# Kernel optimization log

Hardware: AMD Instinct MI355X
Metric: run time of the kernel (lower is better)

## Reference

```python
import jax, jax.numpy as jnp
import numpy as np
import math

B, S, D = 2, 2048, 2048
H, KVH, WIN = 16, 4, 256
HD = D // H            # 128
QPER = H // KVH        # 4


def setup_inputs() -> dict:
    key = jax.random.key(0)
    ks = jax.random.split(key, 9)
    s = lambda k, shp: jax.random.normal(k, shp, dtype=jnp.float32) * 0.02
    return {
        "x": jax.random.normal(ks[0], (B, S, D), dtype=jnp.float32),
        "Wq": s(ks[1], (D, D)),            "bq": jnp.zeros((D,), jnp.float32),
        "Wk": s(ks[2], (D, KVH * HD)),      "bk": jnp.zeros((KVH * HD,), jnp.float32),
        "Wv": s(ks[3], (D, KVH * HD)),      "bv": jnp.zeros((KVH * HD,), jnp.float32),
        "Wo": s(ks[4], (D, D)),            "bo": jnp.zeros((D,), jnp.float32),
    }


def reference(x, Wq, bq, Wk, bk, Wv, bv, Wo, bo):
    b, s, _ = x.shape
    # projections
    Q = (x @ Wq + bq).reshape(b, s, H, HD).transpose(0, 2, 1, 3)     # [b,H,s,hd]
    K = (x @ Wk + bk).reshape(b, s, KVH, HD).transpose(0, 2, 1, 3)   # [b,kvh,s,hd]
    V = (x @ Wv + bv).reshape(b, s, KVH, HD).transpose(0, 2, 1, 3)   # [b,kvh,s,hd]
    # GQA grouping: head h = g*QPER + q
    Qg = Q.reshape(b, KVH, QPER, s, HD)                               # [b,g,q,s,hd]
    scores = jnp.einsum('bgqsd,bgtd->bgqst', Qg, K)                   # [b,g,q,s,s]
    i = jnp.arange(s)[:, None]
    j = jnp.arange(s)[None, :]
    keep = (j <= i) & (j >= i - WIN + 1)                              # [s,s]
    scores = jnp.where(keep, scores, -jnp.inf)
    A = jax.nn.softmax(scores / math.sqrt(HD), axis=-1)
    O = jnp.einsum('bgqst,bgtd->bgqsd', A, V)                         # [b,g,q,s,hd]
    O = O.reshape(b, H, s, HD).transpose(0, 2, 1, 3).reshape(b, s, D)
    return O @ Wo + bo
```

## Files before the change

kernel.cpp:

```cpp
#include <hip/hip_runtime.h>
#include <hip/hip_bf16.h>
#include <math.h>

typedef __bf16 bf16_t;
typedef bf16_t bf16x8 __attribute__((ext_vector_type(8)));
typedef bf16_t bf16x4 __attribute__((ext_vector_type(4)));
typedef float  f32x4  __attribute__((ext_vector_type(4)));

#define NB    2
#define SEQ   2048
#define DIM   2048
#define NHEAD 16
#define NKVH  4
#define HDIM  128
#define WINSZ 256
#define KVD   512
#define QKVN  3072
#define MROWS 4096

__device__ __forceinline__ void async_copy16(const void* g, void* lds) {
    __builtin_amdgcn_global_load_lds(
        (const __attribute__((address_space(1))) void*)g,
        (__attribute__((address_space(3))) void*)lds,
        16, 0, 0);
}

__global__ __launch_bounds__(256) void preprocess(
    const float* __restrict__ x,  const float* __restrict__ Wq,
    const float* __restrict__ bq, const float* __restrict__ Wk,
    const float* __restrict__ bk, const float* __restrict__ Wv,
    const float* __restrict__ bv, const float* __restrict__ Wo,
    bf16_t* __restrict__ xb, bf16_t* __restrict__ WqkvT,
    bf16_t* __restrict__ WoT, float* __restrict__ bqkv) {
    __shared__ float tile[32][33];
    const int tid = threadIdx.x;
    int bid = blockIdx.x;
    if (bid < 8192) {
        int i = (bid * 256 + tid) * 4;
        float4 v = *(const float4*)(x + i);
        bf16x4 o;
        o[0] = (bf16_t)v.x; o[1] = (bf16_t)v.y; o[2] = (bf16_t)v.z; o[3] = (bf16_t)v.w;
        *(bf16x4*)(xb + i) = o;
        return;
    }
    bid -= 8192;
    const float* src; bf16_t* dst; int N;
    if (bid < 4096)       { src = Wq; dst = WqkvT;                          N = DIM; }
    else if (bid < 5120)  { src = Wk; dst = WqkvT + (size_t)DIM * DIM;      N = KVD; bid -= 4096; }
    else if (bid < 6144)  { src = Wv; dst = WqkvT + (size_t)(DIM+KVD)*DIM;  N = KVD; bid -= 5120; }
    else if (bid < 10240) { src = Wo; dst = WoT;                            N = DIM; bid -= 6144; }
    else {
        int i = (bid - 10240) * 256 + tid;
        if (i < QKVN) {
            float v = (i < DIM) ? bq[i] : ((i < DIM + KVD) ? bk[i - DIM] : bv[i - DIM - KVD]);
            bqkv[i] = v;
        }
        return;
    }
    const int K = DIM;
    int ntile = N / 32;
    int n0 = (bid % ntile) * 32, k0 = (bid / ntile) * 32;
    int tx = tid & 31, ty = tid >> 5;
    for (int r = ty; r < 32; r += 8)
        tile[r][tx] = src[(size_t)(k0 + r) * N + n0 + tx];
    __syncthreads();
    for (int r = ty; r < 32; r += 8)
        dst[(size_t)(n0 + r) * K + k0 + tx] = (bf16_t)tile[tx][r];
}

template <int BM, int BN, int MPOS, typename OutT, bool VFUSE>
__global__ __launch_bounds__(512, 1) void gemm1b(const bf16_t* __restrict__ A,
                                                 const bf16_t* __restrict__ Bt,
                                                 const float* __restrict__ bias,
                                                 OutT* __restrict__ C,
                                                 bf16_t* __restrict__ vtb,
                                                 int M, int N, int K, float qs, int qcols) {
    constexpr int NPOS = 8 / MPOS;
    constexpr int ASLOTS = BM / 16;
    constexpr int BSLOTS = BN / 16;
    constexpr int MF = BM / MPOS / 16;
    constexpr int NF = BN / NPOS / 16;
    constexpr int AHALF = BM * 32;
    constexpr int BHALF = BN * 32;
    constexpr int BUFSZ = 2 * (AHALF + BHALF);
    __shared__ bf16_t lds[2 * BUFSZ];

    const int tid  = threadIdx.x;
    const int wave = tid >> 6;
    const int lane = tid & 63;
    const int lg = lane >> 4, lc = lane & 15;
    const int wr = wave / NPOS, wc = wave % NPOS;

    const int nbn  = N / BN;
    const int nblk = (M / BM) * nbn;
    const int qq   = nblk >> 3;
    const int swz  = (blockIdx.x & 7) * qq + (blockIdx.x >> 3);
    const long brow = (long)(swz / nbn) * BM;
    const long bcol = (long)(swz % nbn) * BN;

    f32x4 acc[MF][NF] = {};

    auto stage = [&](int buf, int p, int kt) {
        const int kcol = kt * 64 + p * 32;
        const int srow = lane >> 2;
        const int sch  = lane & 3;
        {
            bf16_t* d = lds + buf * BUFSZ + p * AHALF;
#pragma unroll
            for (int s = wave; s < ASLOTS; s += 8) {
                int row = s * 16 + srow;
                int ch  = sch ^ ((row >> 1) & 3);
                async_copy16(A + (brow + row) * (long)K + kcol + ch * 8, d + s * 512);
            }
        }
        {
            bf16_t* d = lds + buf * BUFSZ + 2 * AHALF + p * BHALF;
#pragma unroll
            for (int s = wave; s < BSLOTS; s += 8) {
                int row = s * 16 + srow;
                int ch  = sch ^ ((row >> 1) & 3);
                async_copy16(Bt + (bcol + row) * (long)K + kcol + ch * 8, d + s * 512);
            }
        }
    };

    stage(0, 0, 0);
    stage(0, 1, 0);

    const int NT = K >> 6;
    const int cswz = (lg ^ ((lc >> 1) & 3)) * 8;
    for (int t = 0; t < NT; ++t) {
        asm volatile("s_waitcnt vmcnt(0)" ::: "memory");
        __builtin_amdgcn_s_barrier();
        asm volatile("" ::: "memory");
        const bf16_t* base = lds + (t & 1) * BUFSZ;
#pragma unroll
        for (int p = 0; p < 2; ++p) {
            const bf16_t* Ab = base + p * AHALF;
            const bf16_t* Bb = base + 2 * AHALF + p * BHALF;
            bf16x8 af[MF], bv[NF];
#pragma unroll
            for (int m = 0; m < MF; ++m)
                af[m] = *(const bf16x8*)(Ab + (wr * (BM / MPOS) + m * 16 + lc) * 32 + cswz);
#pragma unroll
            for (int n = 0; n < NF; ++n)
                bv[n] = *(const bf16x8*)(Bb + (wc * (BN / NPOS) + n * 16 + lc) * 32 + cswz);
            if (t + 1 < NT) stage((t + 1) & 1, p, t + 1);
#pragma unroll
            for (int m = 0; m < MF; ++m)
#pragma unroll
                for (int n = 0; n < NF; ++n)
                    acc[m][n] = __builtin_amdgcn_mfma_f32_16x16x32_bf16(af[m], bv[n], acc[m][n], 0, 0, 0);
        }
    }

#pragma unroll
    for (int n = 0; n < NF; ++n) {
        int gc = (int)bcol + wc * (BN / NPOS) + n * 16 + lc;
        float bvs = bias[gc];
        if constexpr (VFUSE) {
            if (gc >= DIM + KVD) {
                int vg = (gc - (DIM + KVD)) >> 7;
                int dl = (gc - (DIM + KVD)) & 127;
#pragma unroll
                for (int m = 0; m < MF; ++m) {
                    long gr = brow + wr * (BM / MPOS) + m * 16 + 4 * lg;
                    int bb = (int)(gr >> 11);
                    int js = (int)(gr & (SEQ - 1));
                    bf16x4 ov;
#pragma unroll
                    for (int r = 0; r < 4; ++r) ov[r] = (bf16_t)(acc[m][n][r] + bvs);
                    *(bf16x4*)(vtb + (((size_t)(bb * NKVH) + vg) * 64 + (js >> 5)) * 4096
                                   + dl * 32 + (js & 31)) = ov;
                }
                continue;
            }
        }
        bool ds = gc < qcols;
#pragma unroll
        for (int m = 0; m < MF; ++m) {
            long gr = brow + wr * (BM / MPOS) + m * 16 + 4 * lg;
#pragma unroll
            for (int r = 0; r < 4; ++r) {
                float v = acc[m][n][r] + bvs;
                if (ds) v *= qs;
                C[(gr + r) * (long)N + gc] = (OutT)v;
            }
        }
    }
}

template <int BM, int BN, typename OutT>
__global__ __launch_bounds__(512, 1) void gemm8p(const bf16_t* __restrict__ A,
                                                 const bf16_t* __restrict__ Bt,
                                                 const float* __restrict__ bias,
                                                 OutT* __restrict__ C,
                                                 int M, int N, int K, float qs, int qcols) {
    constexpr int ASLOTS = BM / 16;
    constexpr int BSLOTS = BN / 16;
    constexpr int MF   = BM / 32;
    constexpr int NF   = BN / 64;
    constexpr int AHALF = BM * 32;
    constexpr int BHALF = BN * 32;
    constexpr int BUFSZ = 2 * (AHALF + BHALF);
    __shared__ bf16_t lds[2 * BUFSZ];

    const int tid  = threadIdx.x;
    const int wave = tid >> 6;
    const int lane = tid & 63;
    const int lg = lane >> 4, lc = lane & 15;
    const int wr = wave >> 2, wc = wave & 3;

    const int nbn  = N / BN;
    const int nblk = (M / BM) * nbn;
    const int qq   = nblk >> 3;
    const int swz  = (blockIdx.x & 7) * qq + (blockIdx.x >> 3);
    const long brow = (long)(swz / nbn) * BM;
    const long bcol = (long)(swz % nbn) * BN;

    const int aiss = (ASLOTS - wave + 7) >> 3;
    const int biss = (BSLOTS - wave + 7) >> 3;
    const int miss = aiss + biss;

    f32x4 acc[MF][NF] = {};

    auto stage = [&](int buf, int p, int kt) {
        const int kcol = kt * 64 + p * 32;
        const int srow = lane >> 2;
        const int sch  = lane & 3;
        {
            bf16_t* d = lds + buf * BUFSZ + p * AHALF;
#pragma unroll
            for (int s = wave; s < ASLOTS; s += 8) {
                int row = s * 16 + srow;
                int ch  = sch ^ ((row >> 1) & 3);
                async_copy16(A + (brow + row) * (long)K + kcol + ch * 8, d + s * 512);
            }
        }
        {
            bf16_t* d = lds + buf * BUFSZ + 2 * AHALF + p * BHALF;
#pragma unroll
            for (int s = wave; s < BSLOTS; s += 8) {
                int row = s * 16 + srow;
                int ch  = sch ^ ((row >> 1) & 3);
                async_copy16(Bt + (bcol + row) * (long)K + kcol + ch * 8, d + s * 512);
            }
        }
    };

    stage(0, 0, 0);
    stage(0, 1, 0);

    const int NT = K >> 6;
    const int cswz = (lg ^ ((lc >> 1) & 3)) * 8;
    for (int t = 0; t < NT; ++t) {
#pragma unroll
        for (int p = 0; p < 2; ++p) {
            if (t == NT - 1 && p == 1) {
                asm volatile("s_waitcnt vmcnt(0)" ::: "memory");
            } else if (miss == 4) {
                asm volatile("s_waitcnt vmcnt(4)" ::: "memory");
            } else if (miss == 3) {
                asm volatile("s_waitcnt vmcnt(3)" ::: "memory");
            } else {
                asm volatile("s_waitcnt vmcnt(2)" ::: "memory");
            }
            __builtin_amdgcn_s_barrier();
            asm volatile("" ::: "memory");
            const bf16_t* Ab = lds + (t & 1) * BUFSZ + p * AHALF;
            const bf16_t* Bb = lds + (t & 1) * BUFSZ + 2 * AHALF + p * BHALF;
            bf16x8 af[MF], bv[NF];
#pragma unroll
            for (int m = 0; m < MF; ++m)
                af[m] = *(const bf16x8*)(Ab + (wr * (BM / 2) + m * 16 + lc) * 32 + cswz);
#pragma unroll
            for (int n = 0; n < NF; ++n)
                bv[n] = *(const bf16x8*)(Bb + (wc * (BN / 4) + n * 16 + lc) * 32 + cswz);
            if (t + 1 < NT) stage((t + 1) & 1, p, t + 1);
            __builtin_amdgcn_s_setprio(1);
#pragma unroll
            for (int m = 0; m < MF; ++m)
#pragma unroll
                for (int n = 0; n < NF; ++n)
                    acc[m][n] = __builtin_amdgcn_mfma_f32_16x16x32_bf16(af[m], bv[n], acc[m][n], 0, 0, 0);
            __builtin_amdgcn_s_setprio(0);
        }
    }

#pragma unroll
    for (int n = 0; n < NF; ++n) {
        int gc = (int)bcol + wc * (BN / 4) + n * 16 + lc;
        float bvs = bias[gc];
        bool ds = gc < qcols;
#pragma unroll
        for (int m = 0; m < MF; ++m) {
            long gr = brow + wr * (BM / 2) + m * 16 + 4 * lg;
#pragma unroll
            for (int r = 0; r < 4; ++r) {
                float v = acc[m][n][r] + bvs;
                if (ds) v *= qs;
                C[(gr + r) * (long)N + gc] = (OutT)v;
            }
        }
    }
}

__global__ __launch_bounds__(256) void attn_kernel(const bf16_t* __restrict__ QKV,
                                                   const bf16_t* __restrict__ Vtb,
                                                   bf16_t* __restrict__ Ob) {
    __shared__ bf16_t Kls[3][32 * 128];
    __shared__ bf16_t Vls[3][128 * 32];
    __shared__ bf16_t Pls[4][32 * 40];

    const int wv   = threadIdx.x >> 6;
    const int lane = threadIdx.x & 63;
    const int lg = lane >> 4, lc = lane & 15;

    const int swb = (blockIdx.x & 7) * 64 + (blockIdx.x >> 3);
    const int ti = swb & 63;
    const int g  = (swb >> 6) & 3;
    const int b  = swb >> 8;
    const int h  = g * 4 + wv;
    const int i0 = ti * 32;
    bf16_t* P = &Pls[wv][0];

    bf16x8 qf[2][4];
#pragma unroll
    for (int sq = 0; sq < 2; ++sq) {
        const bf16_t* qp = QKV + ((size_t)(b * SEQ) + i0 + sq * 16 + lc) * QKVN + h * HDIM + lg * 8;
#pragma unroll
        for (int kk = 0; kk < 4; ++kk) qf[sq][kk] = *(const bf16x8*)(qp + kk * 32);
    }

    auto stage = [&](int buf, int jb) {
        const int j0s = jb * 32;
        const bf16_t* kgb = QKV + ((size_t)(b * SEQ) + j0s) * QKVN + DIM + g * HDIM;
#pragma unroll
        for (int ii = 0; ii < 2; ++ii) {
            int i = wv * 2 + ii;
            int row = i * 4 + (lane >> 4);
            int ch  = (lane & 15) ^ (row & 7);
            async_copy16(kgb + (size_t)row * QKVN + ch * 8, &Kls[buf][i * 512]);
        }
        const bf16_t* vgb = Vtb + (((size_t)(b * NKVH) + g) * 64 + jb) * 4096;
#pragma unroll
        for (int ii = 0; ii < 2; ++ii) {
            int i = wv * 2 + ii;
            int row = i * 16 + (lane >> 2);
            int ch  = (lane & 3) ^ ((row ^ (row >> 2)) & 3);
            async_copy16(vgb + row * 32 + ch * 8, &Vls[buf][i * 512]);
        }
    };

    float m_run[2] = {-1e30f, -1e30f}, l_run[2] = {0.f, 0.f};
    f32x4 oacc[2][8] = {};

    int jlo = i0 - (WINSZ - 1); if (jlo < 0) jlo = 0;
    const int jb0 = jlo >> 5;
    const int jb1 = (i0 + 31) >> 5;

    stage(0, jb0);
    if (jb0 + 1 <= jb1) stage(1, jb0 + 1);

    for (int jb = jb0; jb <= jb1; ++jb) {
        const int j0 = jb * 32;
        const int it = jb - jb0;
        const int cur = it % 3;
        if (jb < jb1) asm volatile("s_waitcnt vmcnt(4)" ::: "memory");
        else          asm volatile("s_waitcnt vmcnt(0)" ::: "memory");
        __builtin_amdgcn_s_barrier();
        asm volatile("" ::: "memory");

        bf16x8 kf[2][4];
#pragma unroll
        for (int t = 0; t < 2; ++t)
#pragma unroll
            for (int kk = 0; kk < 4; ++kk) {
                int row = t * 16 + lc;
                int ch  = (kk * 4 + lg) ^ (row & 7);
                kf[t][kk] = *(const bf16x8*)(&Kls[cur][row * 128 + ch * 8]);
            }
        if (jb + 2 <= jb1) stage((it + 2) % 3, jb + 2);
        asm volatile("s_waitcnt lgkmcnt(0)" ::: "memory");
        __builtin_amdgcn_sched_barrier(0);

        f32x4 s[2][2];
        __builtin_amdgcn_s_setprio(1);
#pragma unroll
        for (int t = 0; t < 2; ++t)
#pragma unroll
            for (int sq = 0; sq < 2; ++sq) {
                f32x4 sv = {};
#pragma unroll
                for (int kk = 0; kk < 4; ++kk)
                    sv = __builtin_amdgcn_mfma_f32_16x16x32_bf16(kf[t][kk], qf[sq][kk], sv, 0, 0, 0);
                s[t][sq] = sv;
            }
        __builtin_amdgcn_s_setprio(0);

        const bool edge = (j0 < i0 - (WINSZ - 32)) || (j0 > i0 - 31);
        if (edge) {
#pragma unroll
            for (int t = 0; t < 2; ++t)
#pragma unroll
                for (int sq = 0; sq < 2; ++sq) {
                    int irow = i0 + sq * 16 + lc;
#pragma unroll
                    for (int r = 0; r < 4; ++r) {
                        int j = j0 + t * 16 + 4 * lg + r;
                        if (j > irow || j < irow - (WINSZ - 1)) s[t][sq][r] = -1e30f;
                    }
                }
        }
        float tmax[2];
#pragma unroll
        for (int sq = 0; sq < 2; ++sq) {
            float tm = fmaxf(fmaxf(fmaxf(s[0][sq][0], s[0][sq][1]), fmaxf(s[0][sq][2], s[0][sq][3])),
                             fmaxf(fmaxf(s[1][sq][0], s[1][sq][1]), fmaxf(s[1][sq][2], s[1][sq][3])));
            tm = fmaxf(tm, __shfl_xor(tm, 16, 64));
            tm = fmaxf(tm, __shfl_xor(tm, 32, 64));
            tmax[sq] = tm;
        }
        if (!__all(tmax[0] - m_run[0] <= 8.0f && tmax[1] - m_run[1] <= 8.0f)) {
#pragma unroll
            for (int sq = 0; sq < 2; ++sq) {
                float m_new = fmaxf(m_run[sq], tmax[sq]);
                float resc = __builtin_amdgcn_exp2f(m_run[sq] - m_new);
                l_run[sq] *= resc;
#pragma unroll
                for (int c = 0; c < 8; ++c) {
                    oacc[sq][c][0] *= resc; oacc[sq][c][1] *= resc;
                    oacc[sq][c][2] *= resc; oacc[sq][c][3] *= resc;
                }
                m_run[sq] = m_new;
            }
        }
        float psum[2] = {0.f, 0.f};
#pragma unroll
        for (int t = 0; t < 2; ++t)
#pragma unroll
            for (int sq = 0; sq < 2; ++sq) {
                bf16x4 pk;
#pragma unroll
                for (int r = 0; r < 4; ++r) {
                    float sv = s[t][sq][r];
                    float p = (edge && sv < -5e29f) ? 0.f : __builtin_amdgcn_exp2f(sv - m_run[sq]);
                    psum[sq] += p;
                    pk[r] = (bf16_t)p;
                }
                *(bf16x4*)(P + (sq * 16 + lc) * 40 + t * 16 + lg * 4) = pk;
            }
#pragma unroll
        for (int sq = 0; sq < 2; ++sq) {
            float ps = psum[sq];
            ps += __shfl_xor(ps, 16, 64);
            ps += __shfl_xor(ps, 32, 64);
            l_run[sq] += ps;
        }
        asm volatile("" ::: "memory");

        bf16x8 vf[8];
#pragma unroll
        for (int c = 0; c < 8; ++c) {
            int row = c * 16 + lc;
            int ch  = lg ^ ((row ^ (row >> 2)) & 3);
            vf[c] = *(const bf16x8*)(&Vls[cur][row * 32 + ch * 8]);
        }
        bf16x8 pf[2];
#pragma unroll
        for (int sq = 0; sq < 2; ++sq)
            pf[sq] = *(const bf16x8*)(P + (sq * 16 + lc) * 40 + lg * 8);

        __builtin_amdgcn_s_setprio(1);
#pragma unroll
        for (int c = 0; c < 8; ++c)
#pragma unroll
            for (int sq = 0; sq < 2; ++sq)
                oacc[sq][c] = __builtin_amdgcn_mfma_f32_16x16x32_bf16(vf[c], pf[sq], oacc[sq][c], 0, 0, 0);
        __builtin_amdgcn_s_setprio(0);
    }

#pragma unroll
    for (int sq = 0; sq < 2; ++sq) {
        const float inv = 1.f / l_run[sq];
#pragma unroll
        for (int c = 0; c < 8; ++c) {
            bf16x4 ov;
#pragma unroll
            for (int r = 0; r < 4; ++r) ov[r] = (bf16_t)(oacc[sq][c][r] * inv);
            *(bf16x4*)(Ob + ((size_t)(b * SEQ) + i0 + sq * 16 + lc) * DIM + h * HDIM + c * 16 + lg * 4) = ov;
        }
    }
}

extern "C" void kernel_launch(void* const* d_in, const int* in_sizes, int n_in,
                              void* d_out, int out_size, void* d_ws, size_t ws_size,
                              hipStream_t stream) {
    const float* x  = (const float*)d_in[0];
    const float* Wq = (const float*)d_in[1];
    const float* bq = (const float*)d_in[2];
    const float* Wk = (const float*)d_in[3];
    const float* bk = (const float*)d_in[4];
    const float* Wv = (const float*)d_in[5];
    const float* bv = (const float*)d_in[6];
    const float* Wo = (const float*)d_in[7];
    const float* bo = (const float*)d_in[8];
    float* out = (float*)d_out;

    char* ws = (char*)d_ws;
    bf16_t* xb    = (bf16_t*)(ws);
    bf16_t* WqkvT = (bf16_t*)(ws + (16u << 20));
    bf16_t* WoT   = (bf16_t*)(ws + (28u << 20));
    bf16_t* QKVb  = (bf16_t*)(ws + (36u << 20));
    float*  bqkv  = (float*) (ws + (60u << 20));
    bf16_t* Vtb   = (bf16_t*)(ws + (61u << 20));
    bf16_t* Ob    = xb;

    const float qs = 0.12751707498038074f;

    preprocess<<<18444, 256, 0, stream>>>(x, Wq, bq, Wk, bk, Wv, bv, Wo,
                                          xb, WqkvT, WoT, bqkv);

    gemm1b<256, 192, 4, bf16_t, true><<<dim3((MROWS / 256) * (QKVN / 192)), 512, 0, stream>>>(
        xb, WqkvT, bqkv, QKVb, Vtb, MROWS, QKVN, DIM, qs, DIM);

    attn_kernel<<<dim3(NB * NKVH * (SEQ / 32)), 256, 0, stream>>>(QKVb, Vtb, Ob);

    gemm8p<128, 256, float><<<dim3((MROWS / 128) * (DIM / 256)), 512, 0, stream>>>(
        Ob, WoT, bo, out, MROWS, DIM, DIM, 1.0f, 0);
}
```

Baseline: 139.7 us.

## Triple-buffer output GEMM and double attention query tile per block

The output-projection GEMM now keeps a three-stage LDS ring, prefetching two k-tiles ahead. It waits at one barrier per k-tile instead of one per half-tile and drops the setprio hints. The attention kernel now runs 8 waves over 64 query rows per block, so each staged K/V tile is shared by two query sub-tiles and per-block K/V loads are halved. The costs are more LDS per GEMM block, extra wasted key blocks at the window edges for the first query sub-tile, and a barrier now shared by 8 waves.

New measurement: 139.0 us, median of 2. About the same (-0.5%).

```diff
diff --git a/kernel.cpp b/kernel.cpp
--- a/kernel.cpp
+++ b/kernel.cpp
@@ -190,26 +190,27 @@
     }
 }
 
-template <int BM, int BN, typename OutT>
-__global__ __launch_bounds__(512, 1) void gemm8p(const bf16_t* __restrict__ A,
-                                                 const bf16_t* __restrict__ Bt,
-                                                 const float* __restrict__ bias,
-                                                 OutT* __restrict__ C,
-                                                 int M, int N, int K, float qs, int qcols) {
+template <int BM, int BN, int MPOS, typename OutT>
+__global__ __launch_bounds__(512, 1) void gemm1b3(const bf16_t* __restrict__ A,
+                                                  const bf16_t* __restrict__ Bt,
+                                                  const float* __restrict__ bias,
+                                                  OutT* __restrict__ C,
+                                                  int M, int N, int K, float qs, int qcols) {
+    constexpr int NPOS = 8 / MPOS;
     constexpr int ASLOTS = BM / 16;
     constexpr int BSLOTS = BN / 16;
-    constexpr int MF   = BM / 32;
-    constexpr int NF   = BN / 64;
+    constexpr int MF = BM / MPOS / 16;
+    constexpr int NF = BN / NPOS / 16;
     constexpr int AHALF = BM * 32;
     constexpr int BHALF = BN * 32;
     constexpr int BUFSZ = 2 * (AHALF + BHALF);
-    __shared__ bf16_t lds[2 * BUFSZ];
+    __shared__ bf16_t lds[3 * BUFSZ];
 
     const int tid  = threadIdx.x;
     const int wave = tid >> 6;
     const int lane = tid & 63;
     const int lg = lane >> 4, lc = lane & 15;
-    const int wr = wave >> 2, wc = wave & 3;
+    const int wr = wave / NPOS, wc = wave % NPOS;
 
     const int nbn  = N / BN;
     const int nblk = (M / BM) * nbn;
@@ -220,7 +221,7 @@
 
     const int aiss = (ASLOTS - wave + 7) >> 3;
     const int biss = (BSLOTS - wave + 7) >> 3;
-    const int miss = aiss + biss;
+    const int m2   = 2 * (aiss + biss);
 
     f32x4 acc[MF][NF] = {};
 
@@ -250,51 +251,47 @@
 
     stage(0, 0, 0);
     stage(0, 1, 0);
+    stage(1, 0, 1);
+    stage(1, 1, 1);
 
     const int NT = K >> 6;
     const int cswz = (lg ^ ((lc >> 1) & 3)) * 8;
     for (int t = 0; t < NT; ++t) {
+        if (t == NT - 1)      asm volatile("s_waitcnt vmcnt(0)" ::: "memory");
+        else if (m2 == 6)     asm volatile("s_waitcnt vmcnt(6)" ::: "memory");
+        else if (m2 == 8)     asm volatile("s_waitcnt vmcnt(8)" ::: "memory");
+        else                  asm volatile("s_waitcnt vmcnt(4)" ::: "memory");
+        __builtin_amdgcn_s_barrier();
+        asm volatile("" ::: "memory");
+        const bf16_t* base = lds + (t % 3) * BUFSZ;
 #pragma unroll
         for (int p = 0; p < 2; ++p) {
-            if (t == NT - 1 && p == 1) {
-                asm volatile("s_waitcnt vmcnt(0)" ::: "memory");
-            } else if (miss == 4) {
-                asm volatile("s_waitcnt vmcnt(4)" ::: "memory");
-            } else if (miss == 3) {
-                asm volatile("s_waitcnt vmcnt(3)" ::: "memory");
-            } else {
-                asm volatile("s_waitcnt vmcnt(2)" ::: "memory");
-            }
-            __builtin_amdgcn_s_barrier();
-            asm volatile("" ::: "memory");
-            const bf16_t* Ab = lds + (t & 1) * BUFSZ + p * AHALF;
-            const bf16_t* Bb = lds + (t & 1) * BUFSZ + 2 * AHALF + p * BHALF;
+            const bf16_t* Ab = base + p * AHALF;
+            const bf16_t* Bb = base + 2 * AHALF + p * BHALF;
             bf16x8 af[MF], bv[NF];
 #pragma unroll
             for (int m = 0; m < MF; ++m)
-                af[m] = *(const bf16x8*)(Ab + (wr * (BM / 2) + m * 16 + lc) * 32 + cswz);
+                af[m] = *(const bf16x8*)(Ab + (wr * (BM / MPOS) + m * 16 + lc) * 32 + cswz);
 #pragma unroll
             for (int n = 0; n < NF; ++n)
-                bv[n] = *(const bf16x8*)(Bb + (wc * (BN / 4) + n * 16 + lc) * 32 + cswz);
-            if (t + 1 < NT) stage((t + 1) & 1, p, t + 1);
-            __builtin_amdgcn_s_setprio(1);
+                bv[n] = *(const bf16x8*)(Bb + (wc * (BN / NPOS) + n * 16 + lc) * 32 + cswz);
+            if (t + 2 < NT) stage((t + 2) % 3, p, t + 2);
 #pragma unroll
             for (int m = 0; m < MF; ++m)
 #pragma unroll
                 for (int n = 0; n < NF; ++n)
                     acc[m][n] = __builtin_amdgcn_mfma_f32_16x16x32_bf16(af[m], bv[n], acc[m][n], 0, 0, 0);
-            __builtin_amdgcn_s_setprio(0);
         }
     }
 
 #pragma unroll
     for (int n = 0; n < NF; ++n) {
-        int gc = (int)bcol + wc * (BN / 4) + n * 16 + lc;
+        int gc = (int)bcol + wc * (BN / NPOS) + n * 16 + lc;
         float bvs = bias[gc];
         bool ds = gc < qcols;
 #pragma unroll
         for (int m = 0; m < MF; ++m) {
-            long gr = brow + wr * (BM / 2) + m * 16 + 4 * lg;
+            long gr = brow + wr * (BM / MPOS) + m * 16 + 4 * lg;
 #pragma unroll
             for (int r = 0; r < 4; ++r) {
                 float v = acc[m][n][r] + bvs;
@@ -305,23 +302,26 @@
     }
 }
 
-__global__ __launch_bounds__(256) void attn_kernel(const bf16_t* __restrict__ QKV,
+__global__ __launch_bounds__(512) void attn_kernel(const bf16_t* __restrict__ QKV,
                                                    const bf16_t* __restrict__ Vtb,
                                                    bf16_t* __restrict__ Ob) {
     __shared__ bf16_t Kls[3][32 * 128];
     __shared__ bf16_t Vls[3][128 * 32];
-    __shared__ bf16_t Pls[4][32 * 40];
+    __shared__ bf16_t Pls[8][32 * 40];
 
     const int wv   = threadIdx.x >> 6;
     const int lane = threadIdx.x & 63;
     const int lg = lane >> 4, lc = lane & 15;
-
-    const int swb = (blockIdx.x & 7) * 64 + (blockIdx.x >> 3);
-    const int ti = swb & 63;
-    const int g  = (swb >> 6) & 3;
-    const int b  = swb >> 8;
-    const int h  = g * 4 + wv;
-    const int i0 = ti * 32;
+    const int wg = wv >> 2;
+    const int hh = wv & 3;
+
+    const int swb = (blockIdx.x & 7) * 32 + (blockIdx.x >> 3);
+    const int ti = swb & 31;
+    const int g  = (swb >> 5) & 3;
+    const int b  = swb >> 7;
+    const int h  = g * 4 + hh;
+    const int i0b = ti * 64;
+    const int i0  = i0b + wg * 32;
     bf16_t* P = &Pls[wv][0];
 
     bf16x8 qf[2][4];
@@ -333,31 +333,26 @@
     }
 
     auto stage = [&](int buf, int jb) {
-        const int j0s = jb * 32;
-        const bf16_t* kgb = QKV + ((size_t)(b * SEQ) + j0s) * QKVN + DIM + g * HDIM;
-#pragma unroll
-        for (int ii = 0; ii < 2; ++ii) {
-            int i = wv * 2 + ii;
-            int row = i * 4 + (lane >> 4);
+        const bf16_t* kgb = QKV + ((size_t)(b * SEQ) + jb * 32) * QKVN + DIM + g * HDIM;
+        {
+            int row = wv * 4 + (lane >> 4);
             int ch  = (lane & 15) ^ (row & 7);
-            async_copy16(kgb + (size_t)row * QKVN + ch * 8, &Kls[buf][i * 512]);
+            async_copy16(kgb + (size_t)row * QKVN + ch * 8, &Kls[buf][wv * 512]);
         }
         const bf16_t* vgb = Vtb + (((size_t)(b * NKVH) + g) * 64 + jb) * 4096;
-#pragma unroll
-        for (int ii = 0; ii < 2; ++ii) {
-            int i = wv * 2 + ii;
-            int row = i * 16 + (lane >> 2);
+        {
+            int row = wv * 16 + (lane >> 2);
             int ch  = (lane & 3) ^ ((row ^ (row >> 2)) & 3);
-            async_copy16(vgb + row * 32 + ch * 8, &Vls[buf][i * 512]);
+            async_copy16(vgb + row * 32 + ch * 8, &Vls[buf][wv * 512]);
         }
     };
 
     float m_run[2] = {-1e30f, -1e30f}, l_run[2] = {0.f, 0.f};
     f32x4 oacc[2][8] = {};
 
-    int jlo = i0 - (WINSZ - 1); if (jlo < 0) jlo = 0;
+    int jlo = i0b - (WINSZ - 1); if (jlo < 0) jlo = 0;
     const int jb0 = jlo >> 5;
-    const int jb1 = (i0 + 31) >> 5;
+    const int jb1 = (i0b + 63) >> 5;
 
     stage(0, jb0);
     if (jb0 + 1 <= jb1) stage(1, jb0 + 1);
@@ -366,7 +361,7 @@
         const int j0 = jb * 32;
         const int it = jb - jb0;
         const int cur = it % 3;
-        if (jb < jb1) asm volatile("s_waitcnt vmcnt(4)" ::: "memory");
+        if (jb < jb1) asm volatile("s_waitcnt vmcnt(2)" ::: "memory");
         else          asm volatile("s_waitcnt vmcnt(0)" ::: "memory");
         __builtin_amdgcn_s_barrier();
         asm volatile("" ::: "memory");
@@ -524,8 +519,8 @@
     gemm1b<256, 192, 4, bf16_t, true><<<dim3((MROWS / 256) * (QKVN / 192)), 512, 0, stream>>>(
         xb, WqkvT, bqkv, QKVb, Vtb, MROWS, QKVN, DIM, qs, DIM);
 
-    attn_kernel<<<dim3(NB * NKVH * (SEQ / 32)), 256, 0, stream>>>(QKVb, Vtb, Ob);
-
-    gemm8p<128, 256, float><<<dim3((MROWS / 128) * (DIM / 256)), 512, 0, stream>>>(
+    attn_kernel<<<dim3(NB * NKVH * (SEQ / 64)), 512, 0, stream>>>(QKVb, Vtb, Ob);
+
+    gemm1b3<128, 256, 2, float><<<dim3((MROWS / 128) * (DIM / 256)), 512, 0, stream>>>(
         Ob, WoT, bo, out, MROWS, DIM, DIM, 1.0f, 0);
 }
```
